# Optimization experiments

Hardware: AMD Instinct MI355X
Metric: run time of the kernel (lower is better)

The kernel has to match this reference:

```python
import jax, jax.numpy as jnp
import numpy as np

DIM = 512
HEADS = 8
TOP_K = 16


def setup_inputs() -> dict:
    key = jax.random.key(0)
    ks = jax.random.split(key, 7)
    B, N, C = 8, 1024, DIM
    std = 0.02
    return {
        "x": jax.random.normal(ks[0], (B, N, C), dtype=jnp.float32),
        "Wq": jax.random.normal(ks[1], (C, C), dtype=jnp.float32) * std,
        "bq": jnp.zeros((C,), dtype=jnp.float32),
        "Wkv": jax.random.normal(ks[2], (C, 2 * C), dtype=jnp.float32) * std,
        "bkv": jnp.zeros((2 * C,), dtype=jnp.float32),
        "Wp": jax.random.normal(ks[3], (C, C), dtype=jnp.float32) * std,
        "bp": jnp.zeros((C,), dtype=jnp.float32),
    }


def reference(x, Wq, bq, Wkv, bkv, Wp, bp):
    B, N, C = x.shape
    H = HEADS
    D = C // H
    scale = D ** (-0.5)

    # q: [B,H,N,D], ReLU-activated
    q = (x @ Wq + bq).reshape(B, N, H, D).transpose(0, 2, 1, 3)
    q = jax.nn.relu(q)
    # kv: [B,N,2,H,D] -> k,v each [B,H,N,D]
    kv = (x @ Wkv + bkv).reshape(B, N, 2, H, D).transpose(2, 0, 3, 1, 4)
    k, v = kv[0], kv[1]

    # dense scores [B,H,N,N]
    attn = jnp.einsum('bhnd,bhmd->bhnm', q, k) * scale

    # top-k mask along last dim (scatter ones at topk indices)
    _, idx = jax.lax.top_k(attn, TOP_K)            # [B,H,N,K]
    flat_attn = attn.reshape(-1, N)
    flat_idx = idx.reshape(-1, TOP_K)
    rows = jnp.arange(flat_attn.shape[0])[:, None]
    mask = jnp.zeros_like(flat_attn).at[rows, flat_idx].set(1.0).reshape(attn.shape)

    # NOTE: faithful to the original - softmax over the full row of attn*mask
    # (masked-out entries contribute exp(0)=1, exactly as in the torch code)
    sparse_attn = jax.nn.softmax(attn * mask, axis=-1)

    out = jnp.einsum('bhnm,bhmd->bhnd', sparse_attn, v)
    out = out.transpose(0, 2, 1, 3).reshape(B, N, C)
    out = out @ Wp + bp
    return out
```

## Files before the change

### kernel.cpp

```cpp
#include <hip/hip_runtime.h>
#include <float.h>

#define BATCH 8
#define SEQ   1024
#define CDIM  512
#define HEADS 8
#define HD    64
#define TOPK  16
#define MTOT  (BATCH*SEQ)

typedef short bf16x8 __attribute__((ext_vector_type(8)));
typedef float f32x4v __attribute__((ext_vector_type(4)));
typedef unsigned int __attribute__((address_space(1))) guint;
typedef unsigned int __attribute__((address_space(3))) luint;

__device__ inline void bf16split(float f, unsigned short& h, unsigned short& l) {
    unsigned u = __float_as_uint(f);
    unsigned hr = (u + 0x7fffu + ((u >> 16) & 1u)) >> 16;
    h = (unsigned short)hr;
    float rest = f - __uint_as_float(hr << 16);
    unsigned v = __float_as_uint(rest);
    l = (unsigned short)((v + 0x7fffu + ((v >> 16) & 1u)) >> 16);
}

__global__ __launch_bounds__(256) void split_x_kernel(
    const float* __restrict__ x,
    unsigned short* __restrict__ xhi, unsigned short* __restrict__ xlo)
{
    size_t i = ((size_t)blockIdx.x * 256 + threadIdx.x) * 4;
    float4 v = *(const float4*)(x + i);
    ushort4 h, l;
    bf16split(v.x, h.x, l.x); bf16split(v.y, h.y, l.y);
    bf16split(v.z, h.z, l.z); bf16split(v.w, h.w, l.w);
    *(ushort4*)(xhi + i) = h;
    *(ushort4*)(xlo + i) = l;
}

__global__ __launch_bounds__(256) void split_wT_kernel(
    const float* __restrict__ Wq, const float* __restrict__ Wkv,
    const float* __restrict__ Wp,
    unsigned short* __restrict__ bThi, unsigned short* __restrict__ bTlo,
    unsigned short* __restrict__ wpThi, unsigned short* __restrict__ wpTlo)
{
    __shared__ float tile[64][65];
    const int ct = blockIdx.x, k0 = blockIdx.y * 64, t = threadIdx.x;
    const float* src; int ld, sc0, dr0;
    unsigned short *dhi, *dlo;
    if (ct < 8)       { src = Wq;  ld = CDIM;     sc0 = ct * 64;        dr0 = ct * 64;              dhi = bThi;  dlo = bTlo;  }
    else if (ct < 24) { src = Wkv; ld = 2 * CDIM; sc0 = (ct - 8) * 64;  dr0 = CDIM + (ct - 8) * 64; dhi = bThi;  dlo = bTlo;  }
    else              { src = Wp;  ld = CDIM;     sc0 = (ct - 24) * 64; dr0 = (ct - 24) * 64;       dhi = wpThi; dlo = wpTlo; }

    #pragma unroll
    for (int i = 0; i < 4; i++) {
        int f = t + i * 256;
        int r = f >> 4, c4 = f & 15;
        float4 v = *(const float4*)(src + (size_t)(k0 + r) * ld + sc0 + c4 * 4);
        tile[c4*4+0][r] = v.x; tile[c4*4+1][r] = v.y;
        tile[c4*4+2][r] = v.z; tile[c4*4+3][r] = v.w;
    }
    __syncthreads();
    #pragma unroll
    for (int i = 0; i < 2; i++) {
        int f = t + i * 256;
        int c = f >> 3, ko = f & 7;
        const float* tp = &tile[c][ko * 8];
        ushort4 h0, l0, h1, l1;
        bf16split(tp[0], h0.x, l0.x); bf16split(tp[1], h0.y, l0.y);
        bf16split(tp[2], h0.z, l0.z); bf16split(tp[3], h0.w, l0.w);
        bf16split(tp[4], h1.x, l1.x); bf16split(tp[5], h1.y, l1.y);
        bf16split(tp[6], h1.z, l1.z); bf16split(tp[7], h1.w, l1.w);
        size_t o = (size_t)(dr0 + c) * CDIM + k0 + ko * 8;
        *(ushort4*)(dhi + o)     = h0; *(ushort4*)(dhi + o + 4) = h1;
        *(ushort4*)(dlo + o)     = l0; *(ushort4*)(dlo + o + 4) = l1;
    }
}

__device__ __forceinline__ void mfma_gemm_core(
    const unsigned short* __restrict__ ahi, const unsigned short* __restrict__ alo,
    const unsigned short* __restrict__ bhi, const unsigned short* __restrict__ blo,
    int row0, int col0, int lane, int w, f32x4v acc[4][4])
{
    __shared__ __align__(16) unsigned short ah_s[2][4096], al_s[2][4096];
    __shared__ __align__(16) unsigned short bh_s[2][4096], bl_s[2][4096];

    const unsigned short* gsrc;
    unsigned short* lb[2];
    if (w == 0)      { gsrc = ahi; lb[0] = ah_s[0]; lb[1] = ah_s[1]; }
    else if (w == 1) { gsrc = alo; lb[0] = al_s[0]; lb[1] = al_s[1]; }
    else if (w == 2) { gsrc = bhi; lb[0] = bh_s[0]; lb[1] = bh_s[1]; }
    else             { gsrc = blo; lb[0] = bl_s[0]; lb[1] = bl_s[1]; }
    const int tile0 = (w < 2) ? row0 : col0;
    const size_t goff = (size_t)(tile0 + (lane & 15)) * CDIM + (lane >> 4) * 8;
    const int wr = w >> 1, wc = w & 1;

    #pragma unroll
    for (int i = 0; i < 4; i++)
        #pragma unroll
        for (int j = 0; j < 4; j++)
            acc[i][j] = (f32x4v){0.f, 0.f, 0.f, 0.f};

    #pragma unroll
    for (int c = 0; c < 8; c++)
        __builtin_amdgcn_global_load_lds(
            (const guint*)(gsrc + goff + (size_t)c * 16 * CDIM),
            (luint*)(lb[0] + c * 512), 16, 0, 0);
    asm volatile("s_waitcnt vmcnt(0)" ::: "memory");
    __builtin_amdgcn_s_barrier();

    int cur = 0;
    for (int kt = 0; kt < CDIM; kt += 32) {
        if (kt + 32 < CDIM) {
            unsigned short* ln = lb[cur ^ 1];
            #pragma unroll
            for (int c = 0; c < 8; c++)
                __builtin_amdgcn_global_load_lds(
                    (const guint*)(gsrc + goff + kt + 32 + (size_t)c * 16 * CDIM),
                    (luint*)(ln + c * 512), 16, 0, 0);
        }

        const unsigned short* ah = ah_s[cur];
        const unsigned short* al = al_s[cur];
        const unsigned short* bh = bh_s[cur];
        const unsigned short* bl = bl_s[cur];
        bf16x8 afh[4], afl[4], bfh[4], bfl[4];
        #pragma unroll
        for (int i = 0; i < 4; i++) {
            afh[i] = *(const bf16x8*)&ah[(((wr*4 + i) * 64) + lane) * 8];
            afl[i] = *(const bf16x8*)&al[(((wr*4 + i) * 64) + lane) * 8];
            bfh[i] = *(const bf16x8*)&bh[(((wc*4 + i) * 64) + lane) * 8];
            bfl[i] = *(const bf16x8*)&bl[(((wc*4 + i) * 64) + lane) * 8];
        }
        #pragma unroll
        for (int i = 0; i < 4; i++)
            #pragma unroll
            for (int j = 0; j < 4; j++) {
                acc[i][j] = __builtin_amdgcn_mfma_f32_16x16x32_bf16(bfh[j], afh[i], acc[i][j], 0, 0, 0);
                acc[i][j] = __builtin_amdgcn_mfma_f32_16x16x32_bf16(bfh[j], afl[i], acc[i][j], 0, 0, 0);
                acc[i][j] = __builtin_amdgcn_mfma_f32_16x16x32_bf16(bfl[j], afh[i], acc[i][j], 0, 0, 0);
            }

        __builtin_amdgcn_sched_barrier(0);
        asm volatile("s_waitcnt vmcnt(0)" ::: "memory");
        __builtin_amdgcn_s_barrier();
        cur ^= 1;
    }
}

__global__ __launch_bounds__(256) void qkv_mfma_kernel(
    const unsigned short* __restrict__ xhi, const unsigned short* __restrict__ xlo,
    const unsigned short* __restrict__ bThi, const unsigned short* __restrict__ bTlo,
    const float* __restrict__ bq, const float* __restrict__ bkv,
    unsigned short* __restrict__ qhi_g, unsigned short* __restrict__ qlo_g,
    unsigned short* __restrict__ khi_g, unsigned short* __restrict__ klo_g,
    float* __restrict__ v_ws)
{
    const int tid = threadIdx.x, lane = tid & 63, w = tid >> 6;
    const int row0 = blockIdx.x * 128, col0 = blockIdx.y * 128;

    f32x4v acc[4][4];
    mfma_gemm_core(xhi, xlo, bThi, bTlo, row0, col0, lane, w, acc);

    const int wr = w >> 1, wc = w & 1;
    const bool isq = (col0 < CDIM);
    #pragma unroll
    for (int i = 0; i < 4; i++) {
        int rG = row0 + (wr*4 + i) * 16 + (lane & 15);
        int bb = rG >> 10, nn = rG & (SEQ - 1);
        #pragma unroll
        for (int j = 0; j < 4; j++) {
            int cG = col0 + (wc*4 + j) * 16 + (lane >> 4) * 4;
            float4 bias4 = isq ? *(const float4*)(bq + cG)
                               : *(const float4*)(bkv + cG - CDIM);
            float4 val;
            val.x = acc[i][j][0] + bias4.x;
            val.y = acc[i][j][1] + bias4.y;
            val.z = acc[i][j][2] + bias4.z;
            val.w = acc[i][j][3] + bias4.w;
            if (isq) {
                val.x = fmaxf(val.x, 0.f); val.y = fmaxf(val.y, 0.f);
                val.z = fmaxf(val.z, 0.f); val.w = fmaxf(val.w, 0.f);
                int hq = cG >> 6, d = cG & 63;
                size_t base = (((size_t)bb * HEADS + hq) * SEQ + nn) * HD + d;
                ushort4 hv, lv;
                bf16split(val.x, hv.x, lv.x); bf16split(val.y, hv.y, lv.y);
                bf16split(val.z, hv.z, lv.z); bf16split(val.w, hv.w, lv.w);
                *(ushort4*)(qhi_g + base) = hv;
                *(ushort4*)(qlo_g + base) = lv;
            } else {
                int c2 = cG - CDIM;
                int t = c2 >> 9, hq = (c2 >> 6) & 7, d = c2 & 63;
                size_t base = (((size_t)bb * HEADS + hq) * SEQ + nn) * HD + d;
                if (t == 0) {
                    ushort4 hv, lv;
                    bf16split(val.x, hv.x, lv.x); bf16split(val.y, hv.y, lv.y);
                    bf16split(val.z, hv.z, lv.z); bf16split(val.w, hv.w, lv.w);
                    *(ushort4*)(khi_g + base) = hv;
                    *(ushort4*)(klo_g + base) = lv;
                } else {
                    *(float4*)(v_ws + base) = val;
                }
            }
        }
    }
}

__global__ __launch_bounds__(256) void vsum_kernel(
    const float* __restrict__ v_ws, float* __restrict__ vsum_ws)
{
    __shared__ float red[4][HD];
    const int bh = blockIdx.x;
    const int d  = threadIdx.x & 63;
    const int sl = threadIdx.x >> 6;
    const float* vh = v_ws + (size_t)bh * SEQ * HD;
    float s = 0.f;
    for (int m = sl * 256; m < (sl + 1) * 256; m++) s += vh[(size_t)m * HD + d];
    red[sl][d] = s;
    __syncthreads();
    if (threadIdx.x < HD)
        vsum_ws[(size_t)bh * HD + d] = red[0][d] + red[1][d] + red[2][d] + red[3][d];
}

__global__ __launch_bounds__(256) void score_kernel(
    const unsigned short* __restrict__ qhi_g, const unsigned short* __restrict__ qlo_g,
    const unsigned short* __restrict__ khi_g, const unsigned short* __restrict__ klo_g,
    float* __restrict__ s_g, int bh0)
{
    __shared__ __align__(16) short qhi_s[4096], qlo_s[4096];
    __shared__ __align__(16) short khi_s[2][4096], klo_s[2][4096];

    const int bhl = blockIdx.y;
    const int bh  = bh0 + bhl;
    const int n0  = blockIdx.x * 64;
    const int tid = threadIdx.x;
    const int lane = tid & 63, w = tid >> 6;
    const int r_st = tid >> 2, c4 = tid & 3;
    const size_t hb = (size_t)bh * SEQ * HD;

    const int s0 = c4 * 2, s1 = s0 + 1;
    const int cx0 = ((r_st >> 4)*2 + (s0 >> 2))*64 + (s0 & 3)*16 + (r_st & 15);
    const int cx1 = ((r_st >> 4)*2 + (s1 >> 2))*64 + (s1 & 3)*16 + (r_st & 15);

    {
        const unsigned short* qp  = qhi_g + hb + (size_t)(n0 + r_st)*HD + c4*16;
        const unsigned short* qp2 = qlo_g + hb + (size_t)(n0 + r_st)*HD + c4*16;
        uint4 h0 = *(const uint4*)qp,  h1 = *(const uint4*)(qp + 8);
        uint4 l0 = *(const uint4*)qp2, l1 = *(const uint4*)(qp2 + 8);
        *(uint4*)&qhi_s[cx0*8] = h0; *(uint4*)&qhi_s[cx1*8] = h1;
        *(uint4*)&qlo_s[cx0*8] = l0; *(uint4*)&qlo_s[cx1*8] = l1;
    }
    __syncthreads();
    bf16x8 qh[2], ql[2];
    #pragma unroll
    for (int h = 0; h < 2; h++) {
        qh[h] = *(bf16x8*)&qhi_s[((w*2 + h)*64 + lane)*8];
        ql[h] = *(bf16x8*)&qlo_s[((w*2 + h)*64 + lane)*8];
    }

    {
        const unsigned short* kp  = khi_g + hb + (size_t)r_st*HD + c4*16;
        const unsigned short* kp2 = klo_g + hb + (size_t)r_st*HD + c4*16;
        uint4 kh0 = *(const uint4*)kp,  kh1 = *(const uint4*)(kp + 8);
        uint4 kl0 = *(const uint4*)kp2, kl1 = *(const uint4*)(kp2 + 8);
        *(uint4*)&khi_s[0][cx0*8] = kh0; *(uint4*)&khi_s[0][cx1*8] = kh1;
        *(uint4*)&klo_s[0][cx0*8] = kl0; *(uint4*)&klo_s[0][cx1*8] = kl1;
    }
    __syncthreads();

    float* srow_base = s_g + ((size_t)bhl << 20);

    for (int mt = 0; mt < SEQ / 64; mt++) {
        const int cur = mt & 1, nxt = cur ^ 1;
        uint4 kh0, kh1, kl0, kl1;
        if (mt + 1 < SEQ / 64) {
            const unsigned short* kp  = khi_g + hb + (size_t)((mt+1)*64 + r_st)*HD + c4*16;
            const unsigned short* kp2 = klo_g + hb + (size_t)((mt+1)*64 + r_st)*HD + c4*16;
            kh0 = *(const uint4*)kp;  kh1 = *(const uint4*)(kp + 8);
            kl0 = *(const uint4*)kp2; kl1 = *(const uint4*)(kp2 + 8);
        }

        #pragma unroll
        for (int ct = 0; ct < 4; ct++) {
            f32x4v acc = {0.f, 0.f, 0.f, 0.f};
            #pragma unroll
            for (int h = 0; h < 2; h++) {
                bf16x8 kfh = *(bf16x8*)&khi_s[cur][((ct*2 + h)*64 + lane)*8];
                bf16x8 kfl = *(bf16x8*)&klo_s[cur][((ct*2 + h)*64 + lane)*8];
                acc = __builtin_amdgcn_mfma_f32_16x16x32_bf16(qh[h], kfh, acc, 0, 0, 0);
                acc = __builtin_amdgcn_mfma_f32_16x16x32_bf16(qh[h], kfl, acc, 0, 0, 0);
                acc = __builtin_amdgcn_mfma_f32_16x16x32_bf16(ql[h], kfh, acc, 0, 0, 0);
            }
            const int col  = mt*64 + ct*16 + (lane & 15);
            const int rowb = n0 + w*16 + (lane >> 4)*4;
            float* sp = srow_base + ((size_t)rowb << 10) + col;
            #pragma unroll
            for (int rg = 0; rg < 4; rg++)
                sp[(size_t)rg << 10] = acc[rg] * 0.125f;
        }

        if (mt + 1 < SEQ / 64) {
            *(uint4*)&khi_s[nxt][cx0*8] = kh0; *(uint4*)&khi_s[nxt][cx1*8] = kh1;
            *(uint4*)&klo_s[nxt][cx0*8] = kl0; *(uint4*)&klo_s[nxt][cx1*8] = kl1;
        }
        __syncthreads();
    }
}

__device__ __forceinline__ unsigned long long packkey(float f, int gidx) {
    unsigned u = __float_as_uint(f);
    unsigned o = u ^ ((unsigned)((int)u >> 31) | 0x80000000u);
    return ((unsigned long long)o << 32) | (unsigned)(~gidx);
}

struct TopCache { unsigned long long t0, t1, t2, t3; int cnt; };

__device__ __forceinline__ void cache_insert(TopCache& c, unsigned long long k) {
    bool b0 = k > c.t0, b1 = k > c.t1, b2 = k > c.t2, b3 = k > c.t3;
    c.t3 = b3 ? (b2 ? c.t2 : k) : c.t3;
    c.t2 = b2 ? (b1 ? c.t1 : k) : c.t2;
    c.t1 = b1 ? (b0 ? c.t0 : k) : c.t1;
    c.t0 = b0 ? k : c.t0;
}

__device__ __forceinline__ void cache_build(TopCache& c, const float* v, int gbase) {
    c.t0 = c.t1 = c.t2 = c.t3 = 0ull;
    #pragma unroll
    for (int j = 0; j < 16; j++) cache_insert(c, packkey(v[j], gbase + j));
    c.cnt = 4;
}

__device__ __forceinline__ void cache_pop_own(TopCache& c, bool own) {
    c.t0 = own ? c.t1 : c.t0;
    c.t1 = own ? c.t2 : c.t1;
    c.t2 = own ? c.t3 : c.t2;
    c.t3 = own ? 0ull : c.t3;
    c.cnt -= own;
}

__device__ __forceinline__ void cache_refill(TopCache& c, const float* v,
                                             int gbase, unsigned long long kw) {
    c.t0 = c.t1 = c.t2 = c.t3 = 0ull;
    int cc = 0;
    #pragma unroll
    for (int j = 0; j < 16; j++) {
        unsigned long long k = packkey(v[j], gbase + j);
        if (k < kw) { cc++; cache_insert(c, k); }
    }
    c.cnt = cc > 4 ? 4 : cc;
}

__device__ __forceinline__ unsigned umax2(unsigned a, unsigned b) { return a > b ? a : b; }

__device__ __forceinline__ unsigned wave_max_ord(unsigned o) {
    unsigned p;
    p = (unsigned)__builtin_amdgcn_update_dpp(0, (int)o, 0xB1, 0xF, 0xF, true); o = umax2(o, p);
    p = (unsigned)__builtin_amdgcn_update_dpp(0, (int)o, 0x4E, 0xF, 0xF, true); o = umax2(o, p);
    p = (unsigned)__builtin_amdgcn_ds_swizzle((int)o, 0x101F); o = umax2(o, p);
    p = (unsigned)__builtin_amdgcn_ds_swizzle((int)o, 0x201F); o = umax2(o, p);
    p = (unsigned)__builtin_amdgcn_ds_swizzle((int)o, 0x401F); o = umax2(o, p);
    p = (unsigned)__shfl_xor((int)o, 32);                      o = umax2(o, p);
    return o;
}

__device__ __forceinline__ float ord_to_float(unsigned o) {
    return __uint_as_float(o ^ ((unsigned)((int)(~o) >> 31) | 0x80000000u));
}

__global__ __launch_bounds__(256) void topk_pv_kernel(
    const float* __restrict__ s_g, const float* __restrict__ v_ws,
    const float* __restrict__ vsum_ws,
    unsigned short* __restrict__ aohi, unsigned short* __restrict__ aolo, int bh0)
{
    const int lane = threadIdx.x & 63;
    const int wid  = (blockIdx.x * 256 + threadIdx.x) >> 6;
    const int bhl  = wid >> 8;
    const int pr   = wid & 255;
    const int n0   = pr * 4;
    const int bh   = bh0 + bhl;
    const int gbase = lane * 16;

    float v[4][16];
    const float* srow0 = s_g + ((size_t)bhl << 20) + ((size_t)n0 << 10) + gbase;
    #pragma unroll
    for (int r = 0; r < 4; r++) {
        #pragma unroll
        for (int i = 0; i < 4; i++) {
            float4 t4 = *(const float4*)(srow0 + r * SEQ + i * 4);
            v[r][i*4+0] = t4.x; v[r][i*4+1] = t4.y;
            v[r][i*4+2] = t4.z; v[r][i*4+3] = t4.w;
        }
    }

    TopCache c[4];
    #pragma unroll
    for (int r = 0; r < 4; r++) cache_build(c[r], v[r], gbase);

    const float* vh = v_ws + ((size_t)bh << 16);
    const float vs = vsum_ws[(bh << 6) + lane];

    float mx[4], e[4], Z[4], S[4];

    {
        unsigned m[4]; int sl4[4]; unsigned lo[4];
        #pragma unroll
        for (int r = 0; r < 4; r++) m[r] = wave_max_ord((unsigned)(c[r].t0 >> 32));
        #pragma unroll
        for (int r = 0; r < 4; r++) {
            unsigned long long bl = __ballot((unsigned)(c[r].t0 >> 32) == m[r]);
            sl4[r] = __ffsll(bl) - 1;
        }
        #pragma unroll
        for (int r = 0; r < 4; r++)
            lo[r] = (unsigned)__builtin_amdgcn_readlane((int)(unsigned)c[r].t0, sl4[r]);
        #pragma unroll
        for (int r = 0; r < 4; r++) {
            float val = ord_to_float(m[r]);
            int idx = (int)((~lo[r]) & 1023u);
            mx[r] = fmaxf(val, 0.f); e[r] = __expf(-mx[r]);
            float wE = __expf(val - mx[r]);
            Z[r] = (float)(SEQ - TOPK) * e[r] + wE;
            S[r] = (wE - e[r]) * vh[((size_t)idx << 6) + lane];
            cache_pop_own(c[r], lane == sl4[r]);
        }
    }

    #pragma unroll 1
    for (int t = 1; t < TOPK; t++) {
        unsigned m[4]; int sl4[4]; unsigned lo[4];
        #pragma unroll
        for (int r = 0; r < 4; r++) m[r] = wave_max_ord((unsigned)(c[r].t0 >> 32));
        #pragma unroll
        for (int r = 0; r < 4; r++) {
            unsigned long long bl = __ballot((unsigned)(c[r].t0 >> 32) == m[r]);
            sl4[r] = __ffsll(bl) - 1;
        }
        #pragma unroll
        for (int r = 0; r < 4; r++)
            lo[r] = (unsigned)__builtin_amdgcn_readlane((int)(unsigned)c[r].t0, sl4[r]);
        #pragma unroll
        for (int r = 0; r < 4; r++) {
            float val = ord_to_float(m[r]);
            int idx = (int)((~lo[r]) & 1023u);
            float wE = __expf(val - mx[r]);
            Z[r] += wE;
            S[r] = fmaf(wE - e[r], vh[((size_t)idx << 6) + lane], S[r]);
            cache_pop_own(c[r], lane == sl4[r]);
            if (c[r].cnt == 0 && t < TOPK - 1) {
                unsigned long long kw = ((unsigned long long)m[r] << 32) | lo[r];
                cache_refill(c[r], v[r], gbase, kw);
            }
        }
    }

    const int b = bh >> 3, hh = bh & 7;
    size_t o0 = (((size_t)b << 10) + n0) * CDIM + (hh << 6) + lane;
    #pragma unroll
    for (int r = 0; r < 4; r++) {
        float acc = (e[r] * vs + S[r]) / Z[r];
        unsigned short sh, sl;
        bf16split(acc, sh, sl);
        aohi[o0 + (size_t)r * CDIM] = sh;
        aolo[o0 + (size_t)r * CDIM] = sl;
    }
}

__global__ __launch_bounds__(256) void proj_mfma_kernel(
    const unsigned short* __restrict__ aohi, const unsigned short* __restrict__ aolo,
    const unsigned short* __restrict__ wpThi, const unsigned short* __restrict__ wpTlo,
    const float* __restrict__ bp, float* __restrict__ out)
{
    const int tid = threadIdx.x, lane = tid & 63, w = tid >> 6;
    const int row0 = blockIdx.x * 128, col0 = blockIdx.y * 128;

    f32x4v acc[4][4];
    mfma_gemm_core(aohi, aolo, wpThi, wpTlo, row0, col0, lane, w, acc);

    const int wr = w >> 1, wc = w & 1;
    #pragma unroll
    for (int i = 0; i < 4; i++) {
        int rG = row0 + (wr*4 + i) * 16 + (lane & 15);
        #pragma unroll
        for (int j = 0; j < 4; j++) {
            int cG = col0 + (wc*4 + j) * 16 + (lane >> 4) * 4;
            float4 b4 = *(const float4*)(bp + cG);
            float4 val;
            val.x = acc[i][j][0] + b4.x;
            val.y = acc[i][j][1] + b4.y;
            val.z = acc[i][j][2] + b4.z;
            val.w = acc[i][j][3] + b4.w;
            *(float4*)(out + (size_t)rG * CDIM + cG) = val;
        }
    }
}

extern "C" void kernel_launch(void* const* d_in, const int* in_sizes, int n_in,
                              void* d_out, int out_size, void* d_ws, size_t ws_size,
                              hipStream_t stream)
{
    const float* x   = (const float*)d_in[0];
    const float* Wq  = (const float*)d_in[1];
    const float* bq  = (const float*)d_in[2];
    const float* Wkv = (const float*)d_in[3];
    const float* bkv = (const float*)d_in[4];
    const float* Wp  = (const float*)d_in[5];
    const float* bp  = (const float*)d_in[6];
    float* out = (float*)d_out;

    const size_t HSZ = (size_t)BATCH * HEADS * SEQ * HD;
    float* ws    = (float*)d_ws;
    float* v_ws  = ws;
    float* vs_ws = ws + HSZ;
    unsigned short* qhi_g = (unsigned short*)(ws + HSZ + 4096);
    unsigned short* qlo_g = qhi_g + HSZ;
    unsigned short* khi_g = qhi_g + 2 * HSZ;
    unsigned short* klo_g = qhi_g + 3 * HSZ;
    unsigned short* xhi_g = qhi_g + 4 * HSZ;
    unsigned short* xlo_g = qhi_g + 5 * HSZ;
    unsigned short* bThi  = qhi_g + 6 * HSZ;
    unsigned short* bTlo  = bThi + (size_t)1536 * 512;
    unsigned short* wpThi = bThi + (size_t)2 * 1536 * 512;
    unsigned short* wpTlo = wpThi + (size_t)512 * 512;

    const size_t plane_us = 6 * HSZ + (size_t)2 * 1536 * 512 + (size_t)2 * 512 * 512;
    const size_t base_fl  = HSZ + 4096 + plane_us / 2;
    float* s_g = ws + base_fl;

    const size_t avail_fl = (ws_size / 4 > base_fl) ? (ws_size / 4 - base_fl) : 0;
    int G = 32;
    while (G > 1 && (size_t)G * SEQ * SEQ > avail_fl) G >>= 1;

    split_x_kernel<<<dim3((MTOT * CDIM) / (256 * 4)), 256, 0, stream>>>(x, xhi_g, xlo_g);
    split_wT_kernel<<<dim3(32, 8), 256, 0, stream>>>(Wq, Wkv, Wp, bThi, bTlo, wpThi, wpTlo);
    qkv_mfma_kernel<<<dim3(MTOT / 128, 12), 256, 0, stream>>>(
        xhi_g, xlo_g, bThi, bTlo, bq, bkv, qhi_g, qlo_g, khi_g, klo_g, v_ws);
    vsum_kernel<<<BATCH * HEADS, 256, 0, stream>>>(v_ws, vs_ws);
    for (int bh0 = 0; bh0 < BATCH * HEADS; bh0 += G) {
        score_kernel<<<dim3(SEQ / 64, G), 256, 0, stream>>>(
            qhi_g, qlo_g, khi_g, klo_g, s_g, bh0);
        topk_pv_kernel<<<dim3(G * (SEQ / 16)), 256, 0, stream>>>(
            s_g, v_ws, vs_ws, xhi_g, xlo_g, bh0);
    }
    proj_mfma_kernel<<<dim3(MTOT / 128, CDIM / 128), 256, 0, stream>>>(
        xhi_g, xlo_g, wpThi, wpTlo, bp, out);
}
```

Before: 385.9 us.

## Process one score row per wave and batch V gathers after top-k selection

The top-k/PV kernel now assigns one row per wave instead of four, launching four times as many blocks. The selected weights and indices are staged in shared memory, and all sixteen V rows are gathered at the end so the loads can be issued together. Before, each selection step did a dependent load. The aim is to raise occupancy and memory-level parallelism by cutting per-thread register use, at the cost of losing the ILP from interleaving four rows' reductions.

```diff
diff --git a/kernel.cpp b/kernel.cpp
--- a/kernel.cpp
+++ b/kernel.cpp
@@ -370,97 +370,95 @@
     const float* __restrict__ vsum_ws,
     unsigned short* __restrict__ aohi, unsigned short* __restrict__ aolo, int bh0)
 {
+    __shared__ unsigned pair_s[4][TOPK][2];
+
     const int lane = threadIdx.x & 63;
+    const int wv   = threadIdx.x >> 6;
     const int wid  = (blockIdx.x * 256 + threadIdx.x) >> 6;
-    const int bhl  = wid >> 8;
-    const int pr   = wid & 255;
-    const int n0   = pr * 4;
+    const int bhl  = wid >> 10;
+    const int n    = wid & (SEQ - 1);
     const int bh   = bh0 + bhl;
     const int gbase = lane * 16;
 
-    float v[4][16];
-    const float* srow0 = s_g + ((size_t)bhl << 20) + ((size_t)n0 << 10) + gbase;
-    #pragma unroll
-    for (int r = 0; r < 4; r++) {
-        #pragma unroll
-        for (int i = 0; i < 4; i++) {
-            float4 t4 = *(const float4*)(srow0 + r * SEQ + i * 4);
-            v[r][i*4+0] = t4.x; v[r][i*4+1] = t4.y;
-            v[r][i*4+2] = t4.z; v[r][i*4+3] = t4.w;
-        }
-    }
-
-    TopCache c[4];
-    #pragma unroll
-    for (int r = 0; r < 4; r++) cache_build(c[r], v[r], gbase);
-
-    const float* vh = v_ws + ((size_t)bh << 16);
-    const float vs = vsum_ws[(bh << 6) + lane];
-
-    float mx[4], e[4], Z[4], S[4];
+    const float* srow = s_g + ((size_t)bhl << 20) + ((size_t)n << 10) + gbase;
+    float v[16];
+    #pragma unroll
+    for (int i = 0; i < 4; i++) {
+        float4 t4 = *(const float4*)(srow + i * 4);
+        v[i*4+0] = t4.x; v[i*4+1] = t4.y; v[i*4+2] = t4.z; v[i*4+3] = t4.w;
+    }
+
+    TopCache c;
+    cache_build(c, v, gbase);
+
+    float mx, e, Z;
 
     {
-        unsigned m[4]; int sl4[4]; unsigned lo[4];
-        #pragma unroll
-        for (int r = 0; r < 4; r++) m[r] = wave_max_ord((unsigned)(c[r].t0 >> 32));
-        #pragma unroll
-        for (int r = 0; r < 4; r++) {
-            unsigned long long bl = __ballot((unsigned)(c[r].t0 >> 32) == m[r]);
-            sl4[r] = __ffsll(bl) - 1;
-        }
-        #pragma unroll
-        for (int r = 0; r < 4; r++)
-            lo[r] = (unsigned)__builtin_amdgcn_readlane((int)(unsigned)c[r].t0, sl4[r]);
-        #pragma unroll
-        for (int r = 0; r < 4; r++) {
-            float val = ord_to_float(m[r]);
-            int idx = (int)((~lo[r]) & 1023u);
-            mx[r] = fmaxf(val, 0.f); e[r] = __expf(-mx[r]);
-            float wE = __expf(val - mx[r]);
-            Z[r] = (float)(SEQ - TOPK) * e[r] + wE;
-            S[r] = (wE - e[r]) * vh[((size_t)idx << 6) + lane];
-            cache_pop_own(c[r], lane == sl4[r]);
-        }
+        unsigned o = (unsigned)(c.t0 >> 32);
+        unsigned m = wave_max_ord(o);
+        unsigned long long bl = __ballot(o == m);
+        int s = __ffsll(bl) - 1;
+        unsigned lo = (unsigned)__builtin_amdgcn_readlane((int)(unsigned)c.t0, s);
+        float val = ord_to_float(m);
+
+        mx = fmaxf(val, 0.f);
+        e  = __expf(-mx);
+        float wE = __expf(val - mx);
+        Z = (float)(SEQ - TOPK) * e + wE;
+        if (lane == 0) {
+            pair_s[wv][0][0] = __float_as_uint(wE);
+            pair_s[wv][0][1] = (~lo) & 1023u;
+        }
+        cache_pop_own(c, lane == s);
     }
 
     #pragma unroll 1
     for (int t = 1; t < TOPK; t++) {
-        unsigned m[4]; int sl4[4]; unsigned lo[4];
-        #pragma unroll
-        for (int r = 0; r < 4; r++) m[r] = wave_max_ord((unsigned)(c[r].t0 >> 32));
-        #pragma unroll
-        for (int r = 0; r < 4; r++) {
-            unsigned long long bl = __ballot((unsigned)(c[r].t0 >> 32) == m[r]);
-            sl4[r] = __ffsll(bl) - 1;
-        }
-        #pragma unroll
-        for (int r = 0; r < 4; r++)
-            lo[r] = (unsigned)__builtin_amdgcn_readlane((int)(unsigned)c[r].t0, sl4[r]);
-        #pragma unroll
-        for (int r = 0; r < 4; r++) {
-            float val = ord_to_float(m[r]);
-            int idx = (int)((~lo[r]) & 1023u);
-            float wE = __expf(val - mx[r]);
-            Z[r] += wE;
-            S[r] = fmaf(wE - e[r], vh[((size_t)idx << 6) + lane], S[r]);
-            cache_pop_own(c[r], lane == sl4[r]);
-            if (c[r].cnt == 0 && t < TOPK - 1) {
-                unsigned long long kw = ((unsigned long long)m[r] << 32) | lo[r];
-                cache_refill(c[r], v[r], gbase, kw);
-            }
-        }
-    }
+        unsigned o = (unsigned)(c.t0 >> 32);
+        unsigned m = wave_max_ord(o);
+        unsigned long long bl = __ballot(o == m);
+        int s = __ffsll(bl) - 1;
+        unsigned lo = (unsigned)__builtin_amdgcn_readlane((int)(unsigned)c.t0, s);
+        float val = ord_to_float(m);
+
+        float wE = __expf(val - mx);
+        Z += wE;
+        if (lane == 0) {
+            pair_s[wv][t][0] = __float_as_uint(wE);
+            pair_s[wv][t][1] = (~lo) & 1023u;
+        }
+        cache_pop_own(c, lane == s);
+
+        if (c.cnt == 0 && t < TOPK - 1) {
+            unsigned long long kw = ((unsigned long long)m << 32) | lo;
+            cache_refill(c, v, gbase, kw);
+        }
+    }
+
+    float wexp[TOPK]; int mi[TOPK];
+    #pragma unroll
+    for (int t = 0; t < TOPK; t++) {
+        wexp[t] = __uint_as_float(pair_s[wv][t][0]);
+        mi[t]   = (int)pair_s[wv][t][1];
+    }
+    const float* vhp = v_ws + ((size_t)bh << 16);
+    float vr[TOPK];
+    #pragma unroll
+    for (int t = 0; t < TOPK; t++)
+        vr[t] = vhp[((size_t)mi[t] << 6) + lane];
+
+    float acc = e * vsum_ws[(bh << 6) + lane];
+    #pragma unroll
+    for (int t = 0; t < TOPK; t++)
+        acc = fmaf(wexp[t] - e, vr[t], acc);
+    acc /= Z;
 
     const int b = bh >> 3, hh = bh & 7;
-    size_t o0 = (((size_t)b << 10) + n0) * CDIM + (hh << 6) + lane;
-    #pragma unroll
-    for (int r = 0; r < 4; r++) {
-        float acc = (e[r] * vs + S[r]) / Z[r];
-        unsigned short sh, sl;
-        bf16split(acc, sh, sl);
-        aohi[o0 + (size_t)r * CDIM] = sh;
-        aolo[o0 + (size_t)r * CDIM] = sl;
-    }
+    size_t oo = (((size_t)b << 10) + n) * CDIM + (hh << 6) + lane;
+    unsigned short sh, sl;
+    bf16split(acc, sh, sl);
+    aohi[oo] = sh;
+    aolo[oo] = sl;
 }
 
 __global__ __launch_bounds__(256) void proj_mfma_kernel(
@@ -536,7 +534,7 @@
     for (int bh0 = 0; bh0 < BATCH * HEADS; bh0 += G) {
         score_kernel<<<dim3(SEQ / 64, G), 256, 0, stream>>>(
             qhi_g, qlo_g, khi_g, klo_g, s_g, bh0);
-        topk_pv_kernel<<<dim3(G * (SEQ / 16)), 256, 0, stream>>>(
+        topk_pv_kernel<<<dim3(G * (SEQ / 4)), 256, 0, stream>>>(
             s_g, v_ws, vs_ws, xhi_g, xlo_g, bh0);
     }
     proj_mfma_kernel<<<dim3(MTOT / 128, CDIM / 128), 256, 0, stream>>>(
```

Result: faster. 339.3 us, median of 3 (-12.1%).
